# Kernel optimization log

Measured on AMD Instinct MI355X. Metric: run time of the kernel, lower is better.

## Reference

```python
import jax, jax.numpy as jnp
import numpy as np

# Hyperparameters (from init_kwargs)
N = 100000      # num_nodes
T = 4           # num_edge_type
E = 400000      # edges per type
C = 2           # num_channels
L = 2           # num_layers
W_IN = 128      # input feature dim
D = 64          # node_dim (w_out)
NUM_CLASS = 16
BETA = 0.5
M = 10000       # number of target nodes


def setup_inputs() -> dict:
    key = jax.random.key(0)
    ks = jax.random.split(key, 10)
    glorot = np.sqrt(6.0 / (W_IN + D))
    glorot1 = np.sqrt(6.0 / (C * D + D))
    glorot2 = np.sqrt(6.0 / (D + NUM_CLASS))
    return {
        "X": jax.random.normal(ks[0], (N, W_IN), dtype=jnp.float32),
        "edge_value": jax.random.uniform(ks[1], (T, E), dtype=jnp.float32),
        "conv_weights": 0.1 * jax.random.normal(ks[2], (L, C, T), dtype=jnp.float32),
        "Ws": jax.random.uniform(ks[3], (C, W_IN, D), minval=-glorot, maxval=glorot, dtype=jnp.float32),
        "lin1_w": jax.random.uniform(ks[4], (C * D, D), minval=-glorot1, maxval=glorot1, dtype=jnp.float32),
        "lin1_b": jnp.zeros((D,), dtype=jnp.float32),
        "lin_w": jax.random.uniform(ks[5], (D, NUM_CLASS), minval=-glorot2, maxval=glorot2, dtype=jnp.float32),
        "lin_b": jnp.zeros((NUM_CLASS,), dtype=jnp.float32),
        "edge_index": jax.random.randint(ks[6], (T, 2, E), 0, N),
        "target_x": jax.random.randint(ks[7], (M,), 0, N),
    }


def reference(X, edge_value, conv_weights, Ws, lin1_w, lin1_b, lin_w, lin_b,
              edge_index, target_x):
    # Flatten edge types into one big edge list. torch_sparse.coalesce(op='add')
    # followed by torch.sparse.mm is mathematically a duplicate-summing SpMM,
    # i.e. a segment_sum over destination rows.
    rows = edge_index[:, 0, :].reshape(-1)      # [T*E]
    cols = edge_index[:, 1, :].reshape(-1)      # [T*E]
    vals = edge_value.reshape(-1)               # [T*E]
    type_id = jnp.repeat(jnp.arange(T), E)      # [T*E] edge-type id (constant)

    # Per-channel input projections: X_ = X @ Ws[c]  -> [C, N, D]
    X_ = jnp.einsum('nf,cfd->cnd', X, Ws)
    H = X_

    for l in range(L):
        # FastGTConv: softmax over edge types per channel
        filt = jax.nn.softmax(conv_weights[l], axis=1)   # [C, T]
        newH = []
        for c in range(C):
            v = vals * filt[c, type_id]                  # [T*E] mixed edge weights
            msgs = v[:, None] * H[c][cols]               # gather + scale: [T*E, D]
            newH.append(jax.ops.segment_sum(msgs, rows, num_segments=N))
        H = jnp.stack(newH)                              # [C, N, D]

    # FastGTN tail: relu(beta*X_ + (1-beta)*H), concat channels, linear1
    Hc = jax.nn.relu(BETA * X_ + (1.0 - BETA) * H)       # [C, N, D]
    Hcat = jnp.transpose(Hc, (1, 0, 2)).reshape(N, C * D)
    H_ = Hcat @ lin1_w + lin1_b                          # [N, D]

    # FastGTNs head: logits at target nodes
    return H_[target_x] @ lin_w + lin_b                  # [M, NUM_CLASS]
```

## Files before the change

### kernel.cpp

```cpp
#include <hip/hip_runtime.h>

#define N_NODES   100000
#define T_TYPES   4
#define E_EDGES   400000
#define E4        100000
#define G_TOT     400000
#define C_CH      2
#define W_INF     128
#define DD        64
#define NUM_CLASS 16
#define BETA      0.5f
#define M_TGT     10000

#define NBKT      391
#define BROWS     256
#define BPAD      4864
#define QPAD      672
#define CHUNK_G   1024
#define NPART_BLK 391
#define PROJ_BLK  1563
#define SROUND    1024

static const size_t PLANE2 = (size_t)N_NODES * DD;

typedef __attribute__((ext_vector_type(8))) short short8x;
typedef __attribute__((ext_vector_type(4))) float f32x4;

__device__ __forceinline__ unsigned bf16rne(float x) {
    unsigned u = __float_as_uint(x);
    return (u + 0x7FFFu + ((u >> 16) & 1u)) >> 16;
}
__device__ __forceinline__ unsigned packbf(float a, float b) {
    return bf16rne(a) | (bf16rne(b) << 16);
}
__device__ __forceinline__ float bflo(unsigned u) { return __uint_as_float(u << 16); }
__device__ __forceinline__ float bfhi(unsigned u) { return __uint_as_float(u & 0xFFFF0000u); }

__device__ __forceinline__ void load_filter(const float* cw, int layer,
                                            float* f0, float* f1) {
    float m0 = -1e30f, m1 = -1e30f;
    #pragma unroll
    for (int t = 0; t < T_TYPES; ++t) {
        f0[t] = cw[layer * C_CH * T_TYPES + t];
        f1[t] = cw[layer * C_CH * T_TYPES + T_TYPES + t];
        m0 = fmaxf(m0, f0[t]); m1 = fmaxf(m1, f1[t]);
    }
    float s0 = 0.f, s1 = 0.f;
    #pragma unroll
    for (int t = 0; t < T_TYPES; ++t) {
        f0[t] = __expf(f0[t] - m0); s0 += f0[t];
        f1[t] = __expf(f1[t] - m1); s1 += f1[t];
    }
    #pragma unroll
    for (int t = 0; t < T_TYPES; ++t) { f0[t] /= s0; f1[t] /= s1; }
}

__global__ void prep_kernel(const float* __restrict__ Ws,
                            unsigned short* __restrict__ Wsb,
                            int* __restrict__ cursor) {
    int b = blockIdx.x;
    int tid = threadIdx.x;
    if (b < 64) {
        int idx = b * 256 + tid;
        int c   = idx >> 13;
        int rem = idx & 8191;
        int d   = rem >> 7;
        int k   = rem & 127;
        Wsb[idx] = (unsigned short)bf16rne(Ws[c * (W_INF * DD) + k * DD + d]);
    } else {
        int idx = (b - 64) * 256 + tid;
        if (idx < NBKT) cursor[idx] = idx * BPAD;
    }
}

__global__ __launch_bounds__(256) void build_proj_kernel(
        const int* __restrict__ edge_index,
        const float* __restrict__ edge_value,
        const float* __restrict__ cw,
        int* __restrict__ cursor,
        int2* __restrict__ edata2,
        const float* __restrict__ X,
        const unsigned short* __restrict__ Wsb,
        unsigned* __restrict__ Xp16) {
    __shared__ int cnt[392];
    __shared__ int lbase[392];
    __shared__ int gbase[392];
    __shared__ int2 le[SROUND];
    __shared__ unsigned short lbk[SROUND];
    int tid = threadIdx.x;

    if (blockIdx.x < NPART_BLK) {
        int p = blockIdx.x;
        for (int j = tid; j < NBKT; j += 256) cnt[j] = 0;
        __syncthreads();

        float f0[T_TYPES], f1[T_TYPES];
        load_filter(cw, 0, f0, f1);

        int px[16], pv[16], rk[16], bk[16];
        int ne = 0;
        #pragma unroll
        for (int g = 0; g < 4; ++g) {
            int idx = p * CHUNK_G + g * 256 + tid;
            if (idx < G_TOT) {
                int t = idx / E4, r = idx - t * E4;
                const int* bptr = edge_index + (size_t)t * 2 * E_EDGES;
                int4   rw = ((const int4*)bptr)[r];
                int4   cl = ((const int4*)(bptr + E_EDGES))[r];
                float4 vv = ((const float4*)(edge_value + (size_t)t * E_EDGES))[r];
                int tb = t << 17;
                int   rr[4] = {rw.x, rw.y, rw.z, rw.w};
                int   cc[4] = {cl.x, cl.y, cl.z, cl.w};
                float vf[4] = {vv.x, vv.y, vv.z, vv.w};
                #pragma unroll
                for (int k = 0; k < 4; ++k) {
                    int b = rr[k] >> 8;
                    px[ne] = cc[k] | tb | ((rr[k] & 255) << 19);
                    pv[ne] = __float_as_int(vf[k]);
                    bk[ne] = b;
                    rk[ne] = atomicAdd(&cnt[b], 1);
                    ++ne;
                }
            }
        }
        __syncthreads();
        if (tid < 64) {
            int c[7]; int s = 0;
            #pragma unroll
            for (int k = 0; k < 7; ++k) {
                int idx = tid * 7 + k;
                c[k] = (idx < NBKT) ? cnt[idx] : 0;
                s += c[k];
            }
            int inc = s;
            #pragma unroll
            for (int off = 1; off < 64; off <<= 1) {
                int v = __shfl_up(inc, off);
                if (tid >= off) inc += v;
            }
            int base = inc - s;
            #pragma unroll
            for (int k = 0; k < 7; ++k) {
                int idx = tid * 7 + k;
                if (idx < NBKT) lbase[idx] = base;
                base += c[k];
            }
        }
        __syncthreads();
        for (int j = tid; j < NBKT; j += 256)
            gbase[j] = cnt[j] ? atomicAdd(&cursor[j], cnt[j]) : 0;
        __syncthreads();

        int ngrp = min(CHUNK_G, G_TOT - p * CHUNK_G);
        int nloc = 4 * ngrp;
        #pragma unroll
        for (int rd = 0; rd < 4; ++rd) {
            int lo = rd * SROUND;
            #pragma unroll
            for (int k = 0; k < 16; ++k) {
                if (k < ne) {
                    int slot = lbase[bk[k]] + rk[k] - lo;
                    if ((unsigned)slot < (unsigned)SROUND) {
                        le[slot]  = make_int2(px[k], pv[k]);
                        lbk[slot] = (unsigned short)bk[k];
                    }
                }
            }
            __syncthreads();
            int nthis = min(SROUND, nloc - lo);
            for (int j = tid; j < nthis; j += 256) {
                int b = lbk[j];
                int2 e = le[j];
                int t = (e.x >> 17) & 3;
                float v = __int_as_float(e.y);
                edata2[gbase[b] + (lo + j - lbase[b])] =
                    make_int2(e.x, (int)packbf(v * f0[t], v * f1[t]));
            }
            __syncthreads();
        }
    } else {
        int row0 = (blockIdx.x - NPART_BLK) * 64;
        int wave = tid >> 6, lane = tid & 63;
        int m = lane & 15, q = lane >> 4;
        int arow = row0 + wave * 16 + m;
        const float4* X4 = (const float4*)X;
        union { short8x s; uint4 u; } A[4];
        bool valid = arow < N_NODES;
        #pragma unroll
        for (int ks = 0; ks < 4; ++ks) {
            float4 va = make_float4(0.f, 0.f, 0.f, 0.f), vb = va;
            if (valid) {
                va = X4[(size_t)arow * 32 + ks * 8 + q * 2];
                vb = X4[(size_t)arow * 32 + ks * 8 + q * 2 + 1];
            }
            A[ks].u = make_uint4(packbf(va.x, va.y), packbf(va.z, va.w),
                                 packbf(vb.x, vb.y), packbf(vb.z, vb.w));
        }

        #pragma unroll
        for (int ct = 0; ct < 4; ++ct) {
            f32x4 acc0 = {0.f, 0.f, 0.f, 0.f};
            f32x4 acc1 = {0.f, 0.f, 0.f, 0.f};
            #pragma unroll
            for (int ks = 0; ks < 4; ++ks) {
                short8x B0 = *(const short8x*)(Wsb + (ct * 16 + m) * 128 + ks * 32 + q * 8);
                short8x B1 = *(const short8x*)(Wsb + 8192 + (ct * 16 + m) * 128 + ks * 32 + q * 8);
                acc0 = __builtin_amdgcn_mfma_f32_16x16x32_bf16(A[ks].s, B0, acc0, 0, 0, 0);
                acc1 = __builtin_amdgcn_mfma_f32_16x16x32_bf16(A[ks].s, B1, acc1, 0, 0, 0);
            }
            #pragma unroll
            for (int r = 0; r < 4; ++r) {
                int row = row0 + wave * 16 + q * 4 + r;
                if (row < N_NODES)
                    Xp16[(size_t)row * DD + ct * 16 + m] = packbf(acc0[r], acc1[r]);
            }
        }
    }
}

__device__ __forceinline__ void qfma(const uint4 h, unsigned wp,
                                     float4& a, float4& b) {
    float w0 = bflo(wp), w1 = bfhi(wp);
    a.x = fmaf(w0, bflo(h.x), a.x);
    a.y = fmaf(w1, bfhi(h.x), a.y);
    a.z = fmaf(w0, bflo(h.y), a.z);
    a.w = fmaf(w1, bfhi(h.y), a.w);
    b.x = fmaf(w0, bflo(h.z), b.x);
    b.y = fmaf(w1, bfhi(h.z), b.y);
    b.z = fmaf(w0, bflo(h.w), b.z);
    b.w = fmaf(w1, bfhi(h.w), b.w);
}

__device__ __forceinline__ void qreduce(float4& a, float4& b) {
    a.x += __shfl_xor(a.x, 16); a.y += __shfl_xor(a.y, 16);
    a.z += __shfl_xor(a.z, 16); a.w += __shfl_xor(a.w, 16);
    b.x += __shfl_xor(b.x, 16); b.y += __shfl_xor(b.y, 16);
    b.z += __shfl_xor(b.z, 16); b.w += __shfl_xor(b.w, 16);
    a.x += __shfl_xor(a.x, 32); a.y += __shfl_xor(a.y, 32);
    a.z += __shfl_xor(a.z, 32); a.w += __shfl_xor(a.w, 32);
    b.x += __shfl_xor(b.x, 32); b.y += __shfl_xor(b.y, 32);
    b.z += __shfl_xor(b.z, 32); b.w += __shfl_xor(b.w, 32);
}

__device__ __forceinline__ int row_beg(const int* offs, int row) {
    return ((row & 31) == 0) ? (row >> 5) * QPAD : offs[row - 1];
}

__global__ __launch_bounds__(256) void sortgather_kernel(
        const int* __restrict__ cursor,
        const int2* __restrict__ edata2,
        int2* __restrict__ edataS,
        int* __restrict__ offs,
        const unsigned* __restrict__ Hin16,
        unsigned* __restrict__ Hout16) {
    __shared__ int rcnt[32];
    __shared__ int rbase[32];
    __shared__ int rcur[32];
    __shared__ int nq;
    __shared__ int2 ls[QPAD];
    __shared__ int2 ls2[QPAD];
    int i = blockIdx.x;
    int b = (i & 7) + ((i >> 6) << 3);
    int o = (i >> 3) & 7;
    if (b >= NBKT) return;
    int tid = threadIdx.x;
    int bb  = b * BPAD;
    int cnt = cursor[b] - bb;

    if (tid < 32) rcnt[tid] = 0;
    if (tid == 0) nq = 0;
    __syncthreads();
    for (int j = tid; j < cnt; j += 256) {
        int2 e = edata2[bb + j];
        int rt = (e.x >> 19) & 255;
        if ((rt >> 5) == o) {
            int pos = atomicAdd(&nq, 1);
            if (pos < QPAD) {
                ls[pos] = e;
                atomicAdd(&rcnt[rt & 31], 1);
            }
        }
    }
    __syncthreads();
    int nl = min(nq, QPAD);
    if (tid < 32) {
        int c = rcnt[tid];
        int inc = c;
        #pragma unroll
        for (int off = 1; off < 32; off <<= 1) {
            int v = __shfl_up(inc, off);
            if (tid >= off) inc += v;
        }
        rbase[tid] = inc - c;
        rcur[tid]  = inc - c;
    }
    __syncthreads();
    for (int j = tid; j < nl; j += 256) {
        int2 e = ls[j];
        int lr = (e.x >> 19) & 31;
        int pos = atomicAdd(&rcur[lr], 1);
        ls2[pos] = e;
    }
    __syncthreads();

    int s  = b * 8 + o;
    int sb = s * QPAD;
    for (int i2 = tid; i2 < nl; i2 += 256)
        edataS[sb + i2] = ls2[i2];
    int row0 = s * 32;
    if (tid < 32 && row0 + tid < N_NODES)
        offs[row0 + tid] = sb + rbase[tid] + rcnt[tid];
    __syncthreads();

    int wv = tid >> 6, lane = tid & 63;
    int s16 = lane & 15, qd = lane >> 4;
    const uint4* hp = (const uint4*)Hin16;
    #pragma unroll
    for (int rr = 0; rr < 2; ++rr) {
        int lr  = wv * 8 + rr * 4 + qd;
        int row = row0 + lr;
        int beg = rbase[lr];
        int end = beg + rcnt[lr];
        float4 a  = make_float4(0.f, 0.f, 0.f, 0.f);
        float4 b4 = make_float4(0.f, 0.f, 0.f, 0.f);
        int i3 = beg;
        for (; i3 + 3 < end; i3 += 4) {
            int2 e0 = ls2[i3], e1 = ls2[i3 + 1], e2 = ls2[i3 + 2], e3 = ls2[i3 + 3];
            uint4 h0 = hp[(size_t)(e0.x & 0x1FFFF) * 16 + s16];
            uint4 h1 = hp[(size_t)(e1.x & 0x1FFFF) * 16 + s16];
            uint4 h2 = hp[(size_t)(e2.x & 0x1FFFF) * 16 + s16];
            uint4 h3 = hp[(size_t)(e3.x & 0x1FFFF) * 16 + s16];
            qfma(h0, (unsigned)e0.y, a, b4);
            qfma(h1, (unsigned)e1.y, a, b4);
            qfma(h2, (unsigned)e2.y, a, b4);
            qfma(h3, (unsigned)e3.y, a, b4);
        }
        if (i3 + 1 < end) {
            int2 e0 = ls2[i3];
            int2 e1 = ls2[i3 + 1];
            uint4 h0 = hp[(size_t)(e0.x & 0x1FFFF) * 16 + s16];
            uint4 h1 = hp[(size_t)(e1.x & 0x1FFFF) * 16 + s16];
            qfma(h0, (unsigned)e0.y, a, b4);
            qfma(h1, (unsigned)e1.y, a, b4);
            i3 += 2;
        }
        if (i3 < end) {
            int2 e = ls2[i3];
            uint4 h = hp[(size_t)(e.x & 0x1FFFF) * 16 + s16];
            qfma(h, (unsigned)e.y, a, b4);
        }
        if (row < N_NODES)
            ((uint4*)Hout16)[(size_t)row * 16 + s16] =
                make_uint4(packbf(a.x, a.y), packbf(a.z, a.w),
                           packbf(b4.x, b4.y), packbf(b4.z, b4.w));
    }
}

__global__ __launch_bounds__(256) void tgt_tail_kernel(
        const unsigned* __restrict__ Hin16,
        const unsigned* __restrict__ Xp16,
        const int* __restrict__ offs,
        const int2* __restrict__ edataS,
        const float* __restrict__ cw,
        const int* __restrict__ tgt,
        const float* __restrict__ lin1_w,
        const float* __restrict__ lin1_b,
        const float* __restrict__ lin_w,
        const float* __restrict__ lin_b,
        float* __restrict__ out) {
    __shared__ float hc[4][W_INF];
    __shared__ float hmid[4][DD];

    int tid = threadIdx.x;

    float f0a[T_TYPES], f1a[T_TYPES], f0b[T_TYPES], f1b[T_TYPES];
    load_filter(cw, 0, f0a, f1a);
    load_filter(cw, 1, f0b, f1b);
    float r0[T_TYPES], r1[T_TYPES];
    #pragma unroll
    for (int t = 0; t < T_TYPES; ++t) { r0[t] = f0b[t] / f0a[t]; r1[t] = f1b[t] / f1a[t]; }

    int w = tid >> 6, lane = tid & 63;
    int s16 = lane & 15, sub = lane >> 4;
    int m = blockIdx.x * 4 + w;
    int row = tgt[m];
    int beg = row_beg(offs, row);
    int end = offs[row];
    const uint4* hp = (const uint4*)Hin16;
    float4 a = make_float4(0.f, 0.f, 0.f, 0.f);
    float4 b = make_float4(0.f, 0.f, 0.f, 0.f);
    for (int i = beg + sub; i < end; i += 4) {
        int2 e = edataS[i];
        int t = (e.x >> 17) & 3;
        uint4 h = hp[(size_t)(e.x & 0x1FFFF) * 16 + s16];
        unsigned wp = (unsigned)e.y;
        float w0 = bflo(wp) * r0[t], w1 = bfhi(wp) * r1[t];
        a.x = fmaf(w0, bflo(h.x), a.x);
        a.y = fmaf(w1, bfhi(h.x), a.y);
        a.z = fmaf(w0, bflo(h.y), a.z);
        a.w = fmaf(w1, bfhi(h.y), a.w);
        b.x = fmaf(w0, bflo(h.z), b.x);
        b.y = fmaf(w1, bfhi(h.z), b.y);
        b.z = fmaf(w0, bflo(h.w), b.z);
        b.w = fmaf(w1, bfhi(h.w), b.w);
    }
    qreduce(a, b);

    if (sub == 0) {
        uint4 xu = ((const uint4*)Xp16)[(size_t)row * 16 + s16];
        int d0 = 4 * s16;
        hc[w][d0 + 0]      = fmaxf(BETA * bflo(xu.x) + (1.f - BETA) * a.x, 0.f);
        hc[w][DD + d0 + 0] = fmaxf(BETA * bfhi(xu.x) + (1.f - BETA) * a.y, 0.f);
        hc[w][d0 + 1]      = fmaxf(BETA * bflo(xu.y) + (1.f - BETA) * a.z, 0.f);
        hc[w][DD + d0 + 1] = fmaxf(BETA * bfhi(xu.y) + (1.f - BETA) * a.w, 0.f);
        hc[w][d0 + 2]      = fmaxf(BETA * bflo(xu.z) + (1.f - BETA) * b.x, 0.f);
        hc[w][DD + d0 + 2] = fmaxf(BETA * bfhi(xu.z) + (1.f - BETA) * b.y, 0.f);
        hc[w][d0 + 3]      = fmaxf(BETA * bflo(xu.w) + (1.f - BETA) * b.z, 0.f);
        hc[w][DD + d0 + 3] = fmaxf(BETA * bfhi(xu.w) + (1.f - BETA) * b.w, 0.f);
    }
    __syncthreads();

    float a1 = lin1_b[lane];
    #pragma unroll 8
    for (int k = 0; k < W_INF; ++k)
        a1 = fmaf(hc[w][k], lin1_w[k * DD + lane], a1);
    hmid[w][lane] = a1;
    __syncthreads();

    if (lane < NUM_CLASS) {
        float o = lin_b[lane];
        #pragma unroll 8
        for (int k = 0; k < DD; ++k)
            o = fmaf(hmid[w][k], lin_w[k * NUM_CLASS + lane], o);
        out[(size_t)m * NUM_CLASS + lane] = o;
    }
}

extern "C" void kernel_launch(void* const* d_in, const int* in_sizes, int n_in,
                              void* d_out, int out_size, void* d_ws, size_t ws_size,
                              hipStream_t stream) {
    const float* X            = (const float*)d_in[0];
    const float* edge_value   = (const float*)d_in[1];
    const float* conv_weights = (const float*)d_in[2];
    const float* Ws           = (const float*)d_in[3];
    const float* lin1_w       = (const float*)d_in[4];
    const float* lin1_b       = (const float*)d_in[5];
    const float* lin_w        = (const float*)d_in[6];
    const float* lin_b        = (const float*)d_in[7];
    const int*   edge_index   = (const int*)d_in[8];
    const int*   target_x     = (const int*)d_in[9];
    float* out = (float*)d_out;

    unsigned*       Xp16 = (unsigned*)d_ws;
    unsigned*       H116 = Xp16 + PLANE2;
    unsigned short* Wsb  = (unsigned short*)(H116 + PLANE2);
    int*            offs = (int*)(Wsb + C_CH * W_INF * DD);
    int*            cursor = offs + N_NODES;
    int2*           edata2 = (int2*)(cursor + 512);
    int2*           edataS = edata2 + (size_t)NBKT * BPAD;

    prep_kernel<<<66, 256, 0, stream>>>(Ws, Wsb, cursor);
    build_proj_kernel<<<NPART_BLK + PROJ_BLK, 256, 0, stream>>>(
        edge_index, edge_value, conv_weights, cursor, edata2, X, Wsb, Xp16);
    sortgather_kernel<<<8 * 392, 256, 0, stream>>>(cursor, edata2, edataS, offs,
                                                   Xp16, H116);
    tgt_tail_kernel<<<M_TGT / 4, 256, 0, stream>>>(H116, Xp16, offs, edataS,
                                                   conv_weights, target_x,
                                                   lin1_w, lin1_b, lin_w, lin_b, out);
}
```

Measured before the change: 240.5 us.

## Compute layer-1 aggregation only for rows feeding target nodes' layer-2

Marks target nodes in a flag array, then during edge partitioning marks source nodes of edges whose destination is a target, and skips the layer-1 gather in sortgather for rows not needed by the final target-only layer-2 computation. This prunes unnecessary SpMM work, since only about 10k targets times their in-degree of source rows are consumed. It adds a memset, extra scattered flag reads and writes in the partition kernel, and an extra prep block range. The result stays exact because the output depends only on target rows.

Result: no change. 243.4 us (+1.2%).

```diff
diff --git a/kernel.cpp b/kernel.cpp
--- a/kernel.cpp
+++ b/kernel.cpp
@@ -20,6 +20,7 @@
 #define NPART_BLK 391
 #define PROJ_BLK  1563
 #define SROUND    1024
+#define NCNT      100032
 
 static const size_t PLANE2 = (size_t)N_NODES * DD;
 
@@ -57,7 +58,9 @@
 
 __global__ void prep_kernel(const float* __restrict__ Ws,
                             unsigned short* __restrict__ Wsb,
-                            int* __restrict__ cursor) {
+                            int* __restrict__ cursor,
+                            const int* __restrict__ tgt,
+                            int* __restrict__ istgt) {
     int b = blockIdx.x;
     int tid = threadIdx.x;
     if (b < 64) {
@@ -67,9 +70,12 @@
         int d   = rem >> 7;
         int k   = rem & 127;
         Wsb[idx] = (unsigned short)bf16rne(Ws[c * (W_INF * DD) + k * DD + d]);
-    } else {
+    } else if (b < 66) {
         int idx = (b - 64) * 256 + tid;
         if (idx < NBKT) cursor[idx] = idx * BPAD;
+    } else {
+        int idx = (b - 66) * 256 + tid;
+        if (idx < M_TGT) istgt[tgt[idx]] = 1;
     }
 }
 
@@ -81,7 +87,9 @@
         int2* __restrict__ edata2,
         const float* __restrict__ X,
         const unsigned short* __restrict__ Wsb,
-        unsigned* __restrict__ Xp16) {
+        unsigned* __restrict__ Xp16,
+        const int* __restrict__ istgt,
+        int* __restrict__ need) {
     __shared__ int cnt[392];
     __shared__ int lbase[392];
     __shared__ int gbase[392];
@@ -169,11 +177,13 @@
             __syncthreads();
             int nthis = min(SROUND, nloc - lo);
             for (int j = tid; j < nthis; j += 256) {
-                int b = lbk[j];
+                int bkt = lbk[j];
                 int2 e = le[j];
                 int t = (e.x >> 17) & 3;
                 float v = __int_as_float(e.y);
-                edata2[gbase[b] + (lo + j - lbase[b])] =
+                int row = (bkt << 8) | ((e.x >> 19) & 255);
+                if (istgt[row]) need[e.x & 0x1FFFF] = 1;
+                edata2[gbase[bkt] + (lo + j - lbase[bkt])] =
                     make_int2(e.x, (int)packbf(v * f0[t], v * f1[t]));
             }
             __syncthreads();
@@ -251,6 +261,7 @@
         const int2* __restrict__ edata2,
         int2* __restrict__ edataS,
         int* __restrict__ offs,
+        const int* __restrict__ need,
         const unsigned* __restrict__ Hin16,
         unsigned* __restrict__ Hout16) {
     __shared__ int rcnt[32];
@@ -319,6 +330,7 @@
     for (int rr = 0; rr < 2; ++rr) {
         int lr  = wv * 8 + rr * 4 + qd;
         int row = row0 + lr;
+        if (row >= N_NODES || !need[row]) continue;
         int beg = rbase[lr];
         int end = beg + rcnt[lr];
         float4 a  = make_float4(0.f, 0.f, 0.f, 0.f);
@@ -349,10 +361,9 @@
             uint4 h = hp[(size_t)(e.x & 0x1FFFF) * 16 + s16];
             qfma(h, (unsigned)e.y, a, b4);
         }
-        if (row < N_NODES)
-            ((uint4*)Hout16)[(size_t)row * 16 + s16] =
-                make_uint4(packbf(a.x, a.y), packbf(a.z, a.w),
-                           packbf(b4.x, b4.y), packbf(b4.z, b4.w));
+        ((uint4*)Hout16)[(size_t)row * 16 + s16] =
+            make_uint4(packbf(a.x, a.y), packbf(a.z, a.w),
+                       packbf(b4.x, b4.y), packbf(b4.z, b4.w));
     }
 }
 
@@ -456,14 +467,18 @@
     unsigned short* Wsb  = (unsigned short*)(H116 + PLANE2);
     int*            offs = (int*)(Wsb + C_CH * W_INF * DD);
     int*            cursor = offs + N_NODES;
-    int2*           edata2 = (int2*)(cursor + 512);
+    int*            istgt  = cursor + 512;
+    int*            need   = istgt + NCNT;
+    int2*           edata2 = (int2*)(need + NCNT);
     int2*           edataS = edata2 + (size_t)NBKT * BPAD;
 
-    prep_kernel<<<66, 256, 0, stream>>>(Ws, Wsb, cursor);
+    hipMemsetAsync(istgt, 0, 2 * NCNT * sizeof(int), stream);
+    prep_kernel<<<106, 256, 0, stream>>>(Ws, Wsb, cursor, target_x, istgt);
     build_proj_kernel<<<NPART_BLK + PROJ_BLK, 256, 0, stream>>>(
-        edge_index, edge_value, conv_weights, cursor, edata2, X, Wsb, Xp16);
+        edge_index, edge_value, conv_weights, cursor, edata2, X, Wsb, Xp16,
+        istgt, need);
     sortgather_kernel<<<8 * 392, 256, 0, stream>>>(cursor, edata2, edataS, offs,
-                                                   Xp16, H116);
+                                                   need, Xp16, H116);
     tgt_tail_kernel<<<M_TGT / 4, 256, 0, stream>>>(H116, Xp16, offs, edataS,
                                                    conv_weights, target_x,
                                                    lin1_w, lin1_b, lin_w, lin_b, out);
```
